# Kernel tuning notes

Measured on AMD Instinct MI355X. Metric: run time of the kernel, lower is better.

The kernel has to match this reference:

```python
import jax, jax.numpy as jnp
import numpy as np

HEADS = 8
DIM_HEAD = 64
GROUPS = 32  # min(dim//4, 32) with dim=256
EPS = 1e-5

def setup_inputs() -> dict:
    key = jax.random.key(0)
    ks = jax.random.split(key, 5)
    C, H, W = 256, 256, 256
    hidden = HEADS * DIM_HEAD  # 512
    x = jax.random.normal(ks[0], (C, H, W), dtype=jnp.float32)
    gn_w = jnp.ones((C,), dtype=jnp.float32)
    gn_b = jnp.zeros((C,), dtype=jnp.float32)
    qkv_w = jax.random.normal(ks[1], (3 * hidden, C), dtype=jnp.float32) * (1.0 / np.sqrt(C))
    qkv_b = jax.random.normal(ks[2], (3 * hidden,), dtype=jnp.float32) * 0.02
    out_w = jax.random.normal(ks[3], (C, hidden), dtype=jnp.float32) * (1.0 / np.sqrt(hidden))
    out_b = jax.random.normal(ks[4], (C,), dtype=jnp.float32) * 0.02
    return {"x": x, "gn_w": gn_w, "gn_b": gn_b, "qkv_w": qkv_w,
            "qkv_b": qkv_b, "out_w": out_w, "out_b": out_b}

def reference(x, gn_w, gn_b, qkv_w, qkv_b, out_w, out_b):
    C, H, W = x.shape
    n = H * W
    # GroupNorm over (channels-in-group, h, w)
    xg = x.reshape(GROUPS, C // GROUPS, H, W)
    mean = xg.mean(axis=(1, 2, 3), keepdims=True)
    var = xg.var(axis=(1, 2, 3), keepdims=True)
    xn = ((xg - mean) * jax.lax.rsqrt(var + EPS)).reshape(C, H, W)
    xn = xn * gn_w[:, None, None] + gn_b[:, None, None]
    # 1x1 conv QKV projection
    qkv = jnp.einsum('oc,chw->ohw', qkv_w, xn) + qkv_b[:, None, None]
    # split as '(qkv heads c) h w -> qkv heads c (h w)'
    q, k, v = qkv.reshape(3, HEADS, DIM_HEAD, n)
    k = jax.nn.softmax(k, axis=-1)  # softmax over spatial axis
    context = jnp.einsum('hdn,hen->hde', k, v)   # [heads, d, d] small
    out = jnp.einsum('hde,hdn->hen', context, q)  # [heads, d, n]
    out = out.reshape(HEADS * DIM_HEAD, H, W)
    # 1x1 conv output projection
    return jnp.einsum('oc,chw->ohw', out_w, out) + out_b[:, None, None]
```

## Files before the change

### kernel.cpp

```cpp
#include <hip/hip_runtime.h>
#include <stdint.h>

typedef __attribute__((ext_vector_type(8))) short bf16x8;
typedef __attribute__((ext_vector_type(4))) float f32x4;
typedef __attribute__((ext_vector_type(4))) unsigned int u32x4;

#define NSP 65536

#define WS_XN     0ULL
#define WS_WFRAG  33554432ULL
#define WS_WEFRAG 34078720ULL
#define WS_PART   34209792ULL
#define WS_AB     34211840ULL
#define WS_CTX    34215936ULL
#define WS_W2     34347008ULL
#define WS_WEFF   35395584ULL
#define WS_BEFF   35657728ULL


__device__ __forceinline__ unsigned short f2bf(float f) {
  union { float f; uint32_t u; } v; v.f = f;
  uint32_t r = v.u + 0x7FFFu + ((v.u >> 16) & 1u);
  return (unsigned short)(r >> 16);
}
__device__ __forceinline__ float bf2f(unsigned short b) {
  union { uint32_t u; float f; } v; v.u = ((uint32_t)b) << 16;
  return v.f;
}

__global__ void k_stats(const float* __restrict__ x, float* __restrict__ part) {
  __shared__ float ss[256], sq[256];
  const int t = threadIdx.x, b = blockIdx.x;
  const f32x4* p = (const f32x4*)(x + (size_t)b * 65536);
  float s = 0.f, qq = 0.f;
  for (int k = 0; k < 64; ++k) {
    f32x4 v = __builtin_nontemporal_load(p + t + 256 * k);
    s  += v[0] + v[1] + v[2] + v[3];
    qq += v[0] * v[0] + v[1] * v[1] + v[2] * v[2] + v[3] * v[3];
  }
  ss[t] = s; sq[t] = qq;
  __syncthreads();
  for (int st = 128; st > 0; st >>= 1) {
    if (t < st) { ss[t] += ss[t + st]; sq[t] += sq[t + st]; }
    __syncthreads();
  }
  if (t == 0) { part[2 * b] = ss[0]; part[2 * b + 1] = sq[0]; }
}

__global__ void k_coef(const float* __restrict__ part, const float* __restrict__ gn_w,
                       const float* __restrict__ gn_b, float* __restrict__ ab) {
  const int c = threadIdx.x;
  const int g = c >> 3;
  float s = 0.f, q = 0.f;
  for (int j = 0; j < 8; ++j) { s += part[(g * 8 + j) * 2]; q += part[(g * 8 + j) * 2 + 1]; }
  const float inv = 1.0f / 524288.0f;
  const float mean = s * inv;
  const float var = q * inv - mean * mean;
  const float rstd = rsqrtf(var + 1e-5f);
  const float a = gn_w[c] * rstd;
  ab[c] = a;
  ab[256 + c] = gn_b[c] - mean * a;
}

__global__ void k_xn(const float* __restrict__ x, const float* __restrict__ ab,
                     unsigned short* __restrict__ xnf) {
  __shared__ float tile[64][66];
  const int t = threadIdx.x;
  const int nb = blockIdx.x, cb = blockIdx.y;
  {
    const int cl = t >> 2, nc = t & 3;
    const int c = cb * 64 + cl;
    const float a = ab[c], b = ab[256 + c];
    const f32x4* src = (const f32x4*)(x + (size_t)c * NSP + nb * 64 + nc * 16);
#pragma unroll
    for (int j = 0; j < 4; ++j) {
      f32x4 v = __builtin_nontemporal_load(src + j);
      v = v * a + b;
      *(f32x4*)&tile[cl][nc * 16 + j * 4] = v;
    }
  }
  __syncthreads();
  {
    const int l = t & 63, w0 = t >> 6;
    u32x4* xnf4 = (u32x4*)xnf;
#pragma unroll
    for (int u2 = 0; u2 < 2; ++u2) {
      const int fp = w0 + u2 * 4;
      const int fl = fp >> 1, ksl = fp & 1;
      union { unsigned short s[8]; u32x4 v; } pk2;
#pragma unroll
      for (int e = 0; e < 8; ++e)
        pk2.s[e] = f2bf(tile[ksl * 32 + (l >> 4) * 8 + e][fl * 16 + (l & 15)]);
      xnf4[((size_t)(nb * 4 + fl) * 8 + cb * 2 + ksl) * 64 + l] = pk2.v;
    }
  }
}

__global__ void k_wfrag(const float* __restrict__ qkv_w, unsigned short* __restrict__ wf) {
  const int blk = blockIdx.x;
  const int l = threadIdx.x;
  const int row = 512 + (blk & 63) * 16 + (l & 15);
  const int c0 = (blk >> 6) * 32 + (l >> 4) * 8;
  const float* src = qkv_w + (size_t)row * 256 + c0;
  union { unsigned short s[8]; u32x4 v; } u;
#pragma unroll
  for (int j = 0; j < 8; ++j) u.s[j] = f2bf(src[j]);
  *(u32x4*)(wf + ((size_t)blk * 64 + l) * 8) = u.v;
}

__launch_bounds__(512, 1)
__global__ void k_kvctx(const unsigned short* __restrict__ xnf,
                        const unsigned short* __restrict__ wfrag,
                        const float* __restrict__ qkv_b,
                        float* __restrict__ sump, float* __restrict__ ctxp) {
  __shared__ __align__(16) char lds[67584];
  const int t = threadIdx.x;
  const int w = t >> 6, l = t & 63;
  const int q = l & 15;
  const int h = blockIdx.x >> 6;
  const int chunk = blockIdx.x & 63;

  {
    const u32x4* wsrc = (const u32x4*)wfrag;
    u32x4* wdst = (u32x4*)lds;
#pragma unroll
    for (int r = 0; r < 8; ++r) {
      const int e = r * 512 + t;
      const int entry = e >> 6, l2 = e & 63;
      const int ph = entry >> 5, ks = (entry >> 2) & 7, jj = entry & 3;
      wdst[e] = wsrc[((size_t)(ks * 64 + ph * 32 + h * 4 + jj)) * 64 + l2];
    }
  }
  __syncthreads();

  const f32x4 fz = {0.f, 0.f, 0.f, 0.f};
  f32x4 ctxa[4][4];
#pragma unroll
  for (int a = 0; a < 4; ++a)
#pragma unroll
    for (int b = 0; b < 4; ++b) ctxa[a][b] = fz;
  float srow[4] = {0.f, 0.f, 0.f, 0.f};
  float bk[4], bv[4];
#pragma unroll
  for (int jj = 0; jj < 4; ++jj) {
    bk[jj] = qkv_b[512 + h * 64 + jj * 16 + q];
    bv[jj] = qkv_b[1024 + h * 64 + jj * 16 + q];
  }

  const u32x4* xnf4 = (const u32x4*)xnf;

  for (int st = 0; st < 4; ++st) {
    const size_t rg0 = (size_t)chunk * 64 + st * 16;
    const u32x4* gA = xnf4 + (rg0 + w) * 512 + l;
    const u32x4* gB = xnf4 + (rg0 + 8 + w) * 512 + l;

    f32x4 ak[2][4] = {{fz, fz, fz, fz}, {fz, fz, fz, fz}};
#pragma unroll
    for (int ks = 0; ks < 8; ++ks) {
      const bf16x8 xaA = *(const bf16x8*)(gA + ks * 64);
      const bf16x8 xaB = *(const bf16x8*)(gB + ks * 64);
#pragma unroll
      for (int jj = 0; jj < 4; ++jj) {
        const bf16x8 bwk = *(const bf16x8*)(lds + ((ks * 4 + jj) * 64 + l) * 16);
        ak[0][jj] = __builtin_amdgcn_mfma_f32_16x16x32_bf16(xaA, bwk, ak[0][jj], 0, 0, 0);
        ak[1][jj] = __builtin_amdgcn_mfma_f32_16x16x32_bf16(xaB, bwk, ak[1][jj], 0, 0, 0);
      }
    }
    bf16x8 pk[4];
#pragma unroll
    for (int jj = 0; jj < 4; ++jj) {
      float s = 0.f;
      bf16x8 p;
#pragma unroll
      for (int r = 0; r < 4; ++r) {
        const unsigned short u0 = f2bf(__expf(ak[0][jj][r] + bk[jj]));
        const unsigned short u1 = f2bf(__expf(ak[1][jj][r] + bk[jj]));
        p[r] = (short)u0; p[r + 4] = (short)u1;
        s += bf2f(u0) + bf2f(u1);
      }
      pk[jj] = p;
      srow[jj] += s;
    }

    asm volatile("" ::: "memory");

    f32x4 av[2][4] = {{fz, fz, fz, fz}, {fz, fz, fz, fz}};
#pragma unroll
    for (int ks = 0; ks < 8; ++ks) {
      const bf16x8 xaA = *(const bf16x8*)(gA + ks * 64);
      const bf16x8 xaB = *(const bf16x8*)(gB + ks * 64);
#pragma unroll
      for (int jj = 0; jj < 4; ++jj) {
        const bf16x8 bwv = *(const bf16x8*)(lds + (((8 + ks) * 4 + jj) * 64 + l) * 16);
        av[0][jj] = __builtin_amdgcn_mfma_f32_16x16x32_bf16(xaA, bwv, av[0][jj], 0, 0, 0);
        av[1][jj] = __builtin_amdgcn_mfma_f32_16x16x32_bf16(xaB, bwv, av[1][jj], 0, 0, 0);
      }
    }
    bf16x8 pv[4];
#pragma unroll
    for (int jj = 0; jj < 4; ++jj) {
      bf16x8 p;
#pragma unroll
      for (int r = 0; r < 4; ++r) {
        p[r]     = (short)f2bf(av[0][jj][r] + bv[jj]);
        p[r + 4] = (short)f2bf(av[1][jj][r] + bv[jj]);
      }
      pv[jj] = p;
    }

#pragma unroll
    for (int ja = 0; ja < 4; ++ja)
#pragma unroll
      for (int jb = 0; jb < 4; ++jb)
        ctxa[ja][jb] = __builtin_amdgcn_mfma_f32_16x16x32_bf16(pk[ja], pv[jb], ctxa[ja][jb], 0, 0, 0);
  }

  __syncthreads();
  {
    float* srl = (float*)(lds + 65536);
#pragma unroll
    for (int jj = 0; jj < 4; ++jj) {
      float s = srow[jj];
      s += __shfl_xor(s, 16, 64);
      s += __shfl_xor(s, 32, 64);
      if (l < 16) srl[w * 64 + jj * 16 + q] = s;
    }
  }
  if (w < 4) {
    float* dw = (float*)lds + w * 4096 + l * 4;
#pragma unroll
    for (int ja = 0; ja < 4; ++ja)
#pragma unroll
      for (int jb = 0; jb < 4; ++jb)
        *(f32x4*)(dw + (ja * 4 + jb) * 256) = ctxa[ja][jb];
  }
  __syncthreads();
  f32x4 part0 = fz, part1 = fz;
  {
    const float* dump = (const float*)lds;
#pragma unroll
    for (int w4 = 0; w4 < 4; ++w4) {
      part0 += *(const f32x4*)(dump + w4 * 4096 + t * 4);
      part1 += *(const f32x4*)(dump + w4 * 4096 + (512 + t) * 4);
    }
  }
  __syncthreads();
  if (w >= 4) {
    float* dw = (float*)lds + (w - 4) * 4096 + l * 4;
#pragma unroll
    for (int ja = 0; ja < 4; ++ja)
#pragma unroll
      for (int jb = 0; jb < 4; ++jb)
        *(f32x4*)(dw + (ja * 4 + jb) * 256) = ctxa[ja][jb];
  }
  __syncthreads();
  {
    const float* dump = (const float*)lds;
#pragma unroll
    for (int w4 = 0; w4 < 4; ++w4) {
      part0 += *(const f32x4*)(dump + w4 * 4096 + t * 4);
      part1 += *(const f32x4*)(dump + w4 * 4096 + (512 + t) * 4);
    }
    float* cp = ctxp + (size_t)blockIdx.x * 4096;
    *(f32x4*)(cp + t * 4) = part0;
    *(f32x4*)(cp + (512 + t) * 4) = part1;
    if (t < 64) {
      const float* srl = (const float*)(lds + 65536);
      float s = 0.f;
#pragma unroll
      for (int w8 = 0; w8 < 8; ++w8) s += srl[w8 * 64 + t];
      sump[(size_t)(h * 64 + t) * 64 + chunk] = s;
    }
  }
}

__global__ void k_ctxred(const float* __restrict__ ctxp, const float* __restrict__ sump,
                         float* __restrict__ ctx, float* __restrict__ sexp) {
  const int t = threadIdx.x;
  if (blockIdx.x < 64) {
    const int m4 = blockIdx.x * 128 + t;
    const int h = m4 >> 10, p4 = m4 & 1023;
    f32x4 s = {0.f, 0.f, 0.f, 0.f};
#pragma unroll 8
    for (int c = 0; c < 64; ++c)
      s += *(const f32x4*)(ctxp + (((size_t)h * 64 + c) * 1024 + p4) * 4);
    const int jajb = p4 >> 6, ll = p4 & 63;
    const int ja = jajb >> 2, jb = jajb & 3;
    const int gg = ll >> 4, qq = ll & 15;
    float* cw = ctx + ((size_t)h * 64 + ja * 16 + gg * 4) * 64 + jb * 16 + qq;
    cw[0] = s[0]; cw[64] = s[1]; cw[128] = s[2]; cw[192] = s[3];
  } else {
    const int r = (blockIdx.x - 64) * 128 + t;
    float s = 0.f;
#pragma unroll 8
    for (int c = 0; c < 64; ++c) s += sump[(size_t)r * 64 + c];
    sexp[r] = s;
  }
}

__global__ void k_w2(const float* __restrict__ out_w, const float* __restrict__ ctx,
                     const float* __restrict__ sexp, float* __restrict__ w2) {
  const int r = blockIdx.x;
  const int h = r >> 6, d = r & 63;
  __shared__ float row[64];
  __shared__ float sinv;
  const int t = threadIdx.x;
  if (t < 64) row[t] = ctx[((size_t)h * 64 + d) * 64 + t];
  if (t == 0) sinv = 1.0f / sexp[r];
  __syncthreads();
  float a = 0.f;
  const float* wp = out_w + (size_t)t * 512 + h * 64;
#pragma unroll 8
  for (int e = 0; e < 64; ++e) a += wp[e] * row[e];
  w2[(size_t)t * 512 + r] = a * sinv;
}

__global__ void k_weff(const float* __restrict__ w2, const float* __restrict__ qkv_w,
                       const float* __restrict__ qkv_b, const float* __restrict__ out_b,
                       float* __restrict__ weff, float* __restrict__ beff) {
  const int o = blockIdx.x;
  const int c = threadIdx.x;
  __shared__ float row[512];
  __shared__ float red[256];
  row[c] = w2[(size_t)o * 512 + c];
  row[256 + c] = w2[(size_t)o * 512 + 256 + c];
  __syncthreads();
  float a = 0.f;
#pragma unroll 8
  for (int r = 0; r < 512; ++r) a += row[r] * qkv_w[(size_t)r * 256 + c];
  weff[o * 256 + c] = a;
  red[c] = row[c] * qkv_b[c] + row[256 + c] * qkv_b[256 + c];
  __syncthreads();
  for (int st = 128; st > 0; st >>= 1) {
    if (c < st) red[c] += red[c + st];
    __syncthreads();
  }
  if (c == 0) beff[o] = out_b[o] + red[0];
}

__global__ void k_wefrag(const float* __restrict__ weff, unsigned short* __restrict__ wf) {
  const int blk = blockIdx.x;
  const int l = threadIdx.x;
  const int row = (blk & 15) * 16 + (l & 15);
  const int c0 = (blk >> 4) * 32 + (l >> 4) * 8;
  const float* src = weff + (size_t)row * 256 + c0;
  union { unsigned short s[8]; u32x4 v; } u;
#pragma unroll
  for (int j = 0; j < 8; ++j) u.s[j] = f2bf(src[j]);
  *(u32x4*)(wf + ((size_t)blk * 64 + l) * 8) = u.v;
}

__launch_bounds__(256, 2)
__global__ void k_final(const unsigned short* __restrict__ xnf,
                        const unsigned short* __restrict__ wef,
                        const float* __restrict__ beff,
                        float* __restrict__ out) {
  __shared__ unsigned short xlds[32768];
  const int t = threadIdx.x;
  const int w = t >> 6, l = t & 63;
  const int q = l & 15, g = l >> 4;
  const int si = w >> 1, sj = w & 1;
  const int bid = (blockIdx.x & 7) * 64 + (blockIdx.x >> 3);
  const size_t n0 = (size_t)bid * 128;
  {
    const u32x4* gs = (const u32x4*)xnf + (size_t)bid * 4096;
    u32x4* ld = (u32x4*)xlds;
#pragma unroll
    for (int k2 = 0; k2 < 16; ++k2)
      ld[t + 256 * k2] = gs[t + 256 * k2];
  }
  __syncthreads();
  const f32x4 fz = {0.f, 0.f, 0.f, 0.f};
  f32x4 acc[4][8];
#pragma unroll
  for (int i = 0; i < 4; ++i)
#pragma unroll
    for (int j = 0; j < 8; ++j) acc[i][j] = fz;
#pragma unroll
  for (int ks = 0; ks < 8; ++ks) {
    bf16x8 xa[4];
#pragma unroll
    for (int i = 0; i < 4; ++i)
      xa[i] = *(const bf16x8*)((const char*)xlds + (((si * 4 + i) * 8 + ks) * 64 + l) * 16);
#pragma unroll
    for (int jj = 0; jj < 8; ++jj) {
      const bf16x8 bw = *(const bf16x8*)(wef + (((size_t)(ks * 16 + sj * 8 + jj)) * 64 + l) * 8);
#pragma unroll
      for (int i = 0; i < 4; ++i)
        acc[i][jj] = __builtin_amdgcn_mfma_f32_16x16x32_bf16(xa[i], bw, acc[i][jj], 0, 0, 0);
    }
  }
  __syncthreads();
  float* trf = (float*)xlds;
#pragma unroll
  for (int k4 = 0; k4 < 4; ++k4) {
    if ((k4 >> 1) == sj) {
#pragma unroll
      for (int jj2 = 0; jj2 < 4; ++jj2) {
        const int jj = (k4 & 1) * 4 + jj2;
        const float be = beff[sj * 128 + jj * 16 + q];
#pragma unroll
        for (int i = 0; i < 4; ++i)
#pragma unroll
          for (int r = 0; r < 4; ++r)
            trf[(jj2 * 16 + q) * 129 + si * 64 + i * 16 + g * 4 + r] = acc[i][jj][r] + be;
      }
    }
    __syncthreads();
#pragma unroll
    for (int j = 0; j < 32; ++j) {
      const int mm = j * 256 + t;
      const int ol = mm >> 7, cc = mm & 127;
      out[(size_t)(k4 * 64 + ol) * NSP + n0 + cc] = trf[ol * 129 + cc];
    }
    __syncthreads();
  }
}

extern "C" void kernel_launch(void* const* d_in, const int* in_sizes, int n_in,
                              void* d_out, int out_size, void* d_ws, size_t ws_size,
                              hipStream_t stream) {
  const float* x     = (const float*)d_in[0];
  const float* gn_w  = (const float*)d_in[1];
  const float* gn_b  = (const float*)d_in[2];
  const float* qkv_w = (const float*)d_in[3];
  const float* qkv_b = (const float*)d_in[4];
  const float* out_w = (const float*)d_in[5];
  const float* out_b = (const float*)d_in[6];
  char* ws = (char*)d_ws;
  unsigned short* xnf = (unsigned short*)(ws + WS_XN);
  unsigned short* wf  = (unsigned short*)(ws + WS_WFRAG);
  unsigned short* wef = (unsigned short*)(ws + WS_WEFRAG);
  float* part   = (float*)(ws + WS_PART);
  float* ab     = (float*)(ws + WS_AB);
  float* ctx    = (float*)(ws + WS_CTX);
  float* w2     = (float*)(ws + WS_W2);
  float* weff   = (float*)(ws + WS_WEFF);
  float* beff   = (float*)(ws + WS_BEFF);
  float* out    = (float*)d_out;
  float* ctxp = (float*)((char*)d_out + 33554432ULL);
  float* sump = (float*)((char*)d_out + 41943040ULL);

  k_wfrag<<<512, 64, 0, stream>>>(qkv_w, wf);
  k_stats<<<256, 256, 0, stream>>>(x, part);
  k_coef<<<1, 256, 0, stream>>>(part, gn_w, gn_b, ab);
  k_xn<<<dim3(1024, 4), 256, 0, stream>>>(x, ab, xnf);
  k_kvctx<<<512, 512, 0, stream>>>(xnf, wf, qkv_b, sump, ctxp);
  k_ctxred<<<68, 128, 0, stream>>>(ctxp, sump, ctx, part);
  k_w2<<<512, 256, 0, stream>>>(out_w, ctx, part, w2);
  k_weff<<<256, 256, 0, stream>>>(w2, qkv_w, qkv_b, out_b, weff, beff);
  k_wefrag<<<128, 64, 0, stream>>>(weff, wef);
  k_final<<<512, 256, 0, stream>>>(xnf, wef, beff, out);
}
```

Baseline: 173.5 us.

## Fold GroupNorm affine into weights and fuse stats with bf16 conversion pass

Removes the separate statistics pass over x by computing per-channel partial sums inside the tile/convert kernel, which now stores raw (un-normalized) x in bf16 fragment layout. The GroupNorm scale is folded into the QKV and effective output weights per input channel, and the shift is folded into new per-row biases (bqv). This saves one full read of the 256 MB input but adds a partial-sum reduction kernel and a bias kernel. Because x is no longer normalized before rounding to bf16, precision may be somewhat lower.

```diff
diff --git a/kernel.cpp b/kernel.cpp
--- a/kernel.cpp
+++ b/kernel.cpp
@@ -16,6 +16,7 @@
 #define WS_W2     34347008ULL
 #define WS_WEFF   35395584ULL
 #define WS_BEFF   35657728ULL
+#define WS_BQV    35658752ULL
 
 
 __device__ __forceinline__ unsigned short f2bf(float f) {
@@ -28,61 +29,34 @@
   return v.f;
 }
 
-__global__ void k_stats(const float* __restrict__ x, float* __restrict__ part) {
-  __shared__ float ss[256], sq[256];
-  const int t = threadIdx.x, b = blockIdx.x;
-  const f32x4* p = (const f32x4*)(x + (size_t)b * 65536);
-  float s = 0.f, qq = 0.f;
-  for (int k = 0; k < 64; ++k) {
-    f32x4 v = __builtin_nontemporal_load(p + t + 256 * k);
-    s  += v[0] + v[1] + v[2] + v[3];
-    qq += v[0] * v[0] + v[1] * v[1] + v[2] * v[2] + v[3] * v[3];
-  }
-  ss[t] = s; sq[t] = qq;
-  __syncthreads();
-  for (int st = 128; st > 0; st >>= 1) {
-    if (t < st) { ss[t] += ss[t + st]; sq[t] += sq[t + st]; }
-    __syncthreads();
-  }
-  if (t == 0) { part[2 * b] = ss[0]; part[2 * b + 1] = sq[0]; }
-}
-
-__global__ void k_coef(const float* __restrict__ part, const float* __restrict__ gn_w,
-                       const float* __restrict__ gn_b, float* __restrict__ ab) {
-  const int c = threadIdx.x;
-  const int g = c >> 3;
-  float s = 0.f, q = 0.f;
-  for (int j = 0; j < 8; ++j) { s += part[(g * 8 + j) * 2]; q += part[(g * 8 + j) * 2 + 1]; }
-  const float inv = 1.0f / 524288.0f;
-  const float mean = s * inv;
-  const float var = q * inv - mean * mean;
-  const float rstd = rsqrtf(var + 1e-5f);
-  const float a = gn_w[c] * rstd;
-  ab[c] = a;
-  ab[256 + c] = gn_b[c] - mean * a;
-}
-
-__global__ void k_xn(const float* __restrict__ x, const float* __restrict__ ab,
-                     unsigned short* __restrict__ xnf) {
+__global__ void k_xnstats(const float* __restrict__ x, unsigned short* __restrict__ xf,
+                          float* __restrict__ p2s, float* __restrict__ p2q) {
   __shared__ float tile[64][66];
   const int t = threadIdx.x;
   const int nb = blockIdx.x, cb = blockIdx.y;
   {
     const int cl = t >> 2, nc = t & 3;
     const int c = cb * 64 + cl;
-    const float a = ab[c], b = ab[256 + c];
     const f32x4* src = (const f32x4*)(x + (size_t)c * NSP + nb * 64 + nc * 16);
+    float s = 0.f, qq = 0.f;
 #pragma unroll
     for (int j = 0; j < 4; ++j) {
       f32x4 v = __builtin_nontemporal_load(src + j);
-      v = v * a + b;
       *(f32x4*)&tile[cl][nc * 16 + j * 4] = v;
+      s  += v[0] + v[1] + v[2] + v[3];
+      qq += v[0] * v[0] + v[1] * v[1] + v[2] * v[2] + v[3] * v[3];
+    }
+    s  += __shfl_xor(s, 1, 64);  s  += __shfl_xor(s, 2, 64);
+    qq += __shfl_xor(qq, 1, 64); qq += __shfl_xor(qq, 2, 64);
+    if (nc == 0) {
+      p2s[(size_t)(cb * 64 + cl) * 1024 + nb] = s;
+      p2q[(size_t)(cb * 64 + cl) * 1024 + nb] = qq;
     }
   }
   __syncthreads();
   {
     const int l = t & 63, w0 = t >> 6;
-    u32x4* xnf4 = (u32x4*)xnf;
+    u32x4* xf4 = (u32x4*)xf;
 #pragma unroll
     for (int u2 = 0; u2 < 2; ++u2) {
       const int fp = w0 + u2 * 4;
@@ -91,12 +65,40 @@
 #pragma unroll
       for (int e = 0; e < 8; ++e)
         pk2.s[e] = f2bf(tile[ksl * 32 + (l >> 4) * 8 + e][fl * 16 + (l & 15)]);
-      xnf4[((size_t)(nb * 4 + fl) * 8 + cb * 2 + ksl) * 64 + l] = pk2.v;
-    }
-  }
-}
-
-__global__ void k_wfrag(const float* __restrict__ qkv_w, unsigned short* __restrict__ wf) {
+      xf4[((size_t)(nb * 4 + fl) * 8 + cb * 2 + ksl) * 64 + l] = pk2.v;
+    }
+  }
+}
+
+__global__ void k_coefg(const float* __restrict__ p2s, const float* __restrict__ p2q,
+                        const float* __restrict__ gn_w, const float* __restrict__ gn_b,
+                        float* __restrict__ ab) {
+  __shared__ float rs[256], rq[256];
+  const int g = blockIdx.x, t = threadIdx.x;
+  const float* ps = p2s + (size_t)g * 8192;
+  const float* pq = p2q + (size_t)g * 8192;
+  float s = 0.f, q = 0.f;
+  for (int i = t; i < 8192; i += 256) { s += ps[i]; q += pq[i]; }
+  rs[t] = s; rq[t] = q;
+  __syncthreads();
+  for (int st = 128; st > 0; st >>= 1) {
+    if (t < st) { rs[t] += rs[t + st]; rq[t] += rq[t + st]; }
+    __syncthreads();
+  }
+  if (t < 8) {
+    const int c = g * 8 + t;
+    const float inv = 1.0f / 524288.0f;
+    const float mean = rs[0] * inv;
+    const float var = rq[0] * inv - mean * mean;
+    const float rstd = rsqrtf(var + 1e-5f);
+    const float a = gn_w[c] * rstd;
+    ab[c] = a;
+    ab[256 + c] = gn_b[c] - mean * a;
+  }
+}
+
+__global__ void k_wfrag(const float* __restrict__ qkv_w, const float* __restrict__ ab,
+                        unsigned short* __restrict__ wf) {
   const int blk = blockIdx.x;
   const int l = threadIdx.x;
   const int row = 512 + (blk & 63) * 16 + (l & 15);
@@ -104,14 +106,30 @@
   const float* src = qkv_w + (size_t)row * 256 + c0;
   union { unsigned short s[8]; u32x4 v; } u;
 #pragma unroll
-  for (int j = 0; j < 8; ++j) u.s[j] = f2bf(src[j]);
+  for (int j = 0; j < 8; ++j) u.s[j] = f2bf(src[j] * ab[c0 + j]);
   *(u32x4*)(wf + ((size_t)blk * 64 + l) * 8) = u.v;
 }
 
+__global__ void k_bkv(const float* __restrict__ qkv_w, const float* __restrict__ qkv_b,
+                      const float* __restrict__ ab, float* __restrict__ bqv) {
+  const int l = threadIdx.x;
+  const int r = blockIdx.x * 4 + (l >> 4);
+  const int li = l & 15;
+  const float* wr = qkv_w + (size_t)r * 256 + li * 16;
+  float s = 0.f;
+#pragma unroll
+  for (int j = 0; j < 16; ++j) s += wr[j] * ab[256 + li * 16 + j];
+  s += __shfl_xor(s, 1, 64);
+  s += __shfl_xor(s, 2, 64);
+  s += __shfl_xor(s, 4, 64);
+  s += __shfl_xor(s, 8, 64);
+  if (li == 0) bqv[r] = qkv_b[r] + s;
+}
+
 __launch_bounds__(512, 1)
-__global__ void k_kvctx(const unsigned short* __restrict__ xnf,
+__global__ void k_kvctx(const unsigned short* __restrict__ xf,
                         const unsigned short* __restrict__ wfrag,
-                        const float* __restrict__ qkv_b,
+                        const float* __restrict__ bqv,
                         float* __restrict__ sump, float* __restrict__ ctxp) {
   __shared__ __align__(16) char lds[67584];
   const int t = threadIdx.x;
@@ -143,16 +161,16 @@
   float bk[4], bv[4];
 #pragma unroll
   for (int jj = 0; jj < 4; ++jj) {
-    bk[jj] = qkv_b[512 + h * 64 + jj * 16 + q];
-    bv[jj] = qkv_b[1024 + h * 64 + jj * 16 + q];
-  }
-
-  const u32x4* xnf4 = (const u32x4*)xnf;
+    bk[jj] = bqv[512 + h * 64 + jj * 16 + q];
+    bv[jj] = bqv[1024 + h * 64 + jj * 16 + q];
+  }
+
+  const u32x4* xf4 = (const u32x4*)xf;
 
   for (int st = 0; st < 4; ++st) {
     const size_t rg0 = (size_t)chunk * 64 + st * 16;
-    const u32x4* gA = xnf4 + (rg0 + w) * 512 + l;
-    const u32x4* gB = xnf4 + (rg0 + 8 + w) * 512 + l;
+    const u32x4* gA = xf4 + (rg0 + w) * 512 + l;
+    const u32x4* gB = xf4 + (rg0 + 8 + w) * 512 + l;
 
     f32x4 ak[2][4] = {{fz, fz, fz, fz}, {fz, fz, fz, fz}};
 #pragma unroll
@@ -316,7 +334,7 @@
 }
 
 __global__ void k_weff(const float* __restrict__ w2, const float* __restrict__ qkv_w,
-                       const float* __restrict__ qkv_b, const float* __restrict__ out_b,
+                       const float* __restrict__ bqv, const float* __restrict__ out_b,
                        float* __restrict__ weff, float* __restrict__ beff) {
   const int o = blockIdx.x;
   const int c = threadIdx.x;
@@ -329,7 +347,7 @@
 #pragma unroll 8
   for (int r = 0; r < 512; ++r) a += row[r] * qkv_w[(size_t)r * 256 + c];
   weff[o * 256 + c] = a;
-  red[c] = row[c] * qkv_b[c] + row[256 + c] * qkv_b[256 + c];
+  red[c] = row[c] * bqv[c] + row[256 + c] * bqv[256 + c];
   __syncthreads();
   for (int st = 128; st > 0; st >>= 1) {
     if (c < st) red[c] += red[c + st];
@@ -338,7 +356,8 @@
   if (c == 0) beff[o] = out_b[o] + red[0];
 }
 
-__global__ void k_wefrag(const float* __restrict__ weff, unsigned short* __restrict__ wf) {
+__global__ void k_wefrag(const float* __restrict__ weff, const float* __restrict__ ab,
+                         unsigned short* __restrict__ wf) {
   const int blk = blockIdx.x;
   const int l = threadIdx.x;
   const int row = (blk & 15) * 16 + (l & 15);
@@ -346,12 +365,12 @@
   const float* src = weff + (size_t)row * 256 + c0;
   union { unsigned short s[8]; u32x4 v; } u;
 #pragma unroll
-  for (int j = 0; j < 8; ++j) u.s[j] = f2bf(src[j]);
+  for (int j = 0; j < 8; ++j) u.s[j] = f2bf(src[j] * ab[c0 + j]);
   *(u32x4*)(wf + ((size_t)blk * 64 + l) * 8) = u.v;
 }
 
 __launch_bounds__(256, 2)
-__global__ void k_final(const unsigned short* __restrict__ xnf,
+__global__ void k_final(const unsigned short* __restrict__ xf,
                         const unsigned short* __restrict__ wef,
                         const float* __restrict__ beff,
                         float* __restrict__ out) {
@@ -363,7 +382,7 @@
   const int bid = (blockIdx.x & 7) * 64 + (blockIdx.x >> 3);
   const size_t n0 = (size_t)bid * 128;
   {
-    const u32x4* gs = (const u32x4*)xnf + (size_t)bid * 4096;
+    const u32x4* gs = (const u32x4*)xf + (size_t)bid * 4096;
     u32x4* ld = (u32x4*)xlds;
 #pragma unroll
     for (int k2 = 0; k2 < 16; ++k2)
@@ -428,27 +447,30 @@
   const float* out_w = (const float*)d_in[5];
   const float* out_b = (const float*)d_in[6];
   char* ws = (char*)d_ws;
-  unsigned short* xnf = (unsigned short*)(ws + WS_XN);
+  unsigned short* xf  = (unsigned short*)(ws + WS_XN);
   unsigned short* wf  = (unsigned short*)(ws + WS_WFRAG);
   unsigned short* wef = (unsigned short*)(ws + WS_WEFRAG);
-  float* part   = (float*)(ws + WS_PART);
+  float* sexp   = (float*)(ws + WS_PART);
   float* ab     = (float*)(ws + WS_AB);
   float* ctx    = (float*)(ws + WS_CTX);
   float* w2     = (float*)(ws + WS_W2);
   float* weff   = (float*)(ws + WS_WEFF);
   float* beff   = (float*)(ws + WS_BEFF);
+  float* bqv    = (float*)(ws + WS_BQV);
   float* out    = (float*)d_out;
   float* ctxp = (float*)((char*)d_out + 33554432ULL);
   float* sump = (float*)((char*)d_out + 41943040ULL);
-
-  k_wfrag<<<512, 64, 0, stream>>>(qkv_w, wf);
-  k_stats<<<256, 256, 0, stream>>>(x, part);
-  k_coef<<<1, 256, 0, stream>>>(part, gn_w, gn_b, ab);
-  k_xn<<<dim3(1024, 4), 256, 0, stream>>>(x, ab, xnf);
-  k_kvctx<<<512, 512, 0, stream>>>(xnf, wf, qkv_b, sump, ctxp);
-  k_ctxred<<<68, 128, 0, stream>>>(ctxp, sump, ctx, part);
-  k_w2<<<512, 256, 0, stream>>>(out_w, ctx, part, w2);
-  k_weff<<<256, 256, 0, stream>>>(w2, qkv_w, qkv_b, out_b, weff, beff);
-  k_wefrag<<<128, 64, 0, stream>>>(weff, wef);
-  k_final<<<512, 256, 0, stream>>>(xnf, wef, beff, out);
-}
+  float* p2s  = (float*)((char*)d_out + 46137344ULL);
+  float* p2q  = (float*)((char*)d_out + 47185920ULL);
+
+  k_xnstats<<<dim3(1024, 4), 256, 0, stream>>>(x, xf, p2s, p2q);
+  k_coefg<<<32, 256, 0, stream>>>(p2s, p2q, gn_w, gn_b, ab);
+  k_wfrag<<<512, 64, 0, stream>>>(qkv_w, ab, wf);
+  k_bkv<<<384, 64, 0, stream>>>(qkv_w, qkv_b, ab, bqv);
+  k_kvctx<<<512, 512, 0, stream>>>(xf, wf, bqv, sump, ctxp);
+  k_ctxred<<<68, 128, 0, stream>>>(ctxp, sump, ctx, sexp);
+  k_w2<<<512, 256, 0, stream>>>(out_w, ctx, sexp, w2);
+  k_weff<<<256, 256, 0, stream>>>(w2, qkv_w, bqv, out_b, weff, beff);
+  k_wefrag<<<128, 64, 0, stream>>>(weff, ab, wef);
+  k_final<<<512, 256, 0, stream>>>(xf, wef, beff, out);
+}
```

New measurement: 172.9 us. About the same (-0.4%).
